# Optimization experiments

Measured on AMD Instinct MI355X. Metric: run time of the kernel, lower is better.

Reference implementation:

```python
import jax, jax.numpy as jnp
import numpy as np

D_MODEL = 2048
NUM_HEADS = 32
NUM_KV_HEADS = 8
HEAD_DIM = D_MODEL // NUM_HEADS  # 64
KV_DIM = NUM_KV_HEADS * HEAD_DIM  # 512


def setup_inputs() -> dict:
    key = jax.random.key(0)
    ks = jax.random.split(key, 9)
    s = 1.0 / np.sqrt(D_MODEL)
    x = jax.random.normal(ks[0], (4, 1024, D_MODEL), dtype=jnp.float32)
    Wq = jax.random.uniform(ks[1], (D_MODEL, D_MODEL), jnp.float32, -s, s)
    bq = jax.random.uniform(ks[2], (D_MODEL,), jnp.float32, -s, s)
    Wk = jax.random.uniform(ks[3], (D_MODEL, KV_DIM), jnp.float32, -s, s)
    bk = jax.random.uniform(ks[4], (KV_DIM,), jnp.float32, -s, s)
    Wv = jax.random.uniform(ks[5], (D_MODEL, KV_DIM), jnp.float32, -s, s)
    bv = jax.random.uniform(ks[6], (KV_DIM,), jnp.float32, -s, s)
    Wo = jax.random.uniform(ks[7], (D_MODEL, D_MODEL), jnp.float32, -s, s)
    bo = jax.random.uniform(ks[8], (D_MODEL,), jnp.float32, -s, s)
    return {"x": x, "Wq": Wq, "bq": bq, "Wk": Wk, "bk": bk,
            "Wv": Wv, "bv": bv, "Wo": Wo, "bo": bo}


def reference(x, Wq, bq, Wk, bk, Wv, bv, Wo, bo):
    B, S, _ = x.shape
    g = NUM_HEADS // NUM_KV_HEADS  # heads per kv head
    # projections
    q = (x @ Wq + bq).reshape(B, S, NUM_HEADS, HEAD_DIM).transpose(0, 2, 1, 3)   # [B,H,S,d]
    k = (x @ Wk + bk).reshape(B, S, NUM_KV_HEADS, HEAD_DIM).transpose(0, 2, 1, 3)  # [B,Hkv,S,d]
    v = (x @ Wv + bv).reshape(B, S, NUM_KV_HEADS, HEAD_DIM).transpose(0, 2, 1, 3)
    # repeat_interleave KV heads across query-head groups
    k = jnp.repeat(k, g, axis=1)  # [B,H,S,d]
    v = jnp.repeat(v, g, axis=1)
    scores = jnp.einsum('bhqd,bhkd->bhqk', q, k) / np.sqrt(HEAD_DIM)  # [B,H,S,S]
    attn = jax.nn.softmax(scores, axis=-1)
    ctx = jnp.einsum('bhqk,bhkd->bhqd', attn, v)  # [B,H,S,d]
    ctx = ctx.transpose(0, 2, 1, 3).reshape(B, S, D_MODEL)
    return ctx @ Wo + bo
```

## Files before the change

### kernel.cpp

```cpp
#include <hip/hip_runtime.h>
#include <stdint.h>

typedef unsigned short u16;
typedef __attribute__((ext_vector_type(8))) __bf16 bf16x8;
typedef __attribute__((ext_vector_type(4))) __bf16 bf16x4;
typedef __attribute__((ext_vector_type(4))) float f32x4;

#define QSCALE 0.1803368801111204f

#if __has_builtin(__builtin_amdgcn_exp2f)
#define EXP2(x) __builtin_amdgcn_exp2f(x)
#else
#define EXP2(x) exp2f(x)
#endif

__device__ __forceinline__ u16 f2bf(float f) {
  uint32_t u = __float_as_uint(f);
  u += 0x7fffu + ((u >> 16) & 1u);
  return (u16)(u >> 16);
}
__device__ __forceinline__ float bf2f(u16 h) {
  return __uint_as_float(((uint32_t)h) << 16);
}
__device__ __forceinline__ uint32_t pack2bf(float a, float b) {
  return (uint32_t)f2bf(a) | ((uint32_t)f2bf(b) << 16);
}

__device__ __forceinline__ void gl_lds16(const u16* g, u16* l) {
  __builtin_amdgcn_global_load_lds(
      (const __attribute__((address_space(1))) unsigned int*)g,
      (__attribute__((address_space(3))) unsigned int*)l, 16, 0, 0);
}

#define S_BAR() __builtin_amdgcn_s_barrier()
#define LGKM0() do { __asm__ volatile("s_waitcnt lgkmcnt(0)" ::: "memory"); \
                     __builtin_amdgcn_sched_barrier(0); } while (0)
#define VMC(N) do { __asm__ volatile("s_waitcnt vmcnt(" #N ")" ::: "memory"); \
                    __builtin_amdgcn_sched_barrier(0); } while (0)

__global__ void detect_dtype(const u16* __restrict__ x, int* __restrict__ flag) {
  __shared__ int any_huge;
  if (threadIdx.x == 0) any_huge = 0;
  __syncthreads();
  int huge = 0;
  for (int i = threadIdx.x; i < 4096; i += 256) {
    float v = bf2f(x[i]);
    if (!(fabsf(v) < 1e6f)) huge = 1;
  }
  if (huge) any_huge = 1;
  __syncthreads();
  if (threadIdx.x == 0) *flag = any_huge;
}

__global__ __launch_bounds__(256) void prep(
    const void* __restrict__ Wq, const void* __restrict__ Wk,
    const void* __restrict__ Wv, const void* __restrict__ Wo,
    const void* __restrict__ x,
    const void* __restrict__ bq, const void* __restrict__ bk,
    const void* __restrict__ bv, const void* __restrict__ bo,
    u16* __restrict__ WT, u16* __restrict__ WoT, u16* __restrict__ xb,
    float* __restrict__ biasf, const int* __restrict__ flag) {
  const int fl = *flag;
  int id = blockIdx.x;
  const int tid = threadIdx.x;
  if (id < 2560) {
    __shared__ u16 tile[64 * 72];
    const void* in; u16* outp; int N, rowoff;
    if (id < 1024)      { in = Wq; outp = WT;  N = 2048; rowoff = 0; }
    else if (id < 1280) { in = Wk; outp = WT;  N = 512;  rowoff = 2048; id -= 1024; }
    else if (id < 1536) { in = Wv; outp = WT;  N = 512;  rowoff = 2560; id -= 1280; }
    else                { in = Wo; outp = WoT; N = 2048; rowoff = 0;    id -= 1536; }
    int tiles_x = N >> 6;
    int nb = (id % tiles_x) * 64, kb = (id / tiles_x) * 64;
    const int kbase = (tid >> 4) * 4, nc = (tid & 15) * 4;
    if (fl) {
      float4 L[4];
#pragma unroll
      for (int p = 0; p < 4; ++p)
        L[p] = *(const float4*)&((const float*)in)[(size_t)(kb + kbase + p) * N + nb + nc];
#pragma unroll
      for (int nj = 0; nj < 4; ++nj) {
        uint2 w;
        w.x = pack2bf(((const float*)&L[0])[nj], ((const float*)&L[1])[nj]);
        w.y = pack2bf(((const float*)&L[2])[nj], ((const float*)&L[3])[nj]);
        *(uint2*)&tile[(nc + nj) * 72 + kbase] = w;
      }
    } else {
      uint2 L[4];
#pragma unroll
      for (int p = 0; p < 4; ++p)
        L[p] = *(const uint2*)&((const u16*)in)[(size_t)(kb + kbase + p) * N + nb + nc];
#pragma unroll
      for (int nj = 0; nj < 4; ++nj) {
        uint2 w;
        w.x = (uint32_t)((const u16*)&L[0])[nj] | ((uint32_t)((const u16*)&L[1])[nj] << 16);
        w.y = (uint32_t)((const u16*)&L[2])[nj] | ((uint32_t)((const u16*)&L[3])[nj] << 16);
        *(uint2*)&tile[(nc + nj) * 72 + kbase] = w;
      }
    }
    __syncthreads();
#pragma unroll
    for (int it = 0; it < 2; ++it) {
      int sid = it * 256 + tid;
      int row = sid >> 3, kseg = (sid & 7) * 8;
      uint4 v = *(const uint4*)&tile[row * 72 + kseg];
      *(uint4*)&outp[(size_t)(rowoff + nb + row) * 2048 + kb + kseg] = v;
    }
  } else if (id < 4608) {
    size_t base = ((size_t)(id - 2560) * 256 + tid) * 16;
    if (fl) {
      const float* xf = (const float*)x;
      float4 a = *(const float4*)&xf[base];
      float4 b = *(const float4*)&xf[base + 4];
      float4 c = *(const float4*)&xf[base + 8];
      float4 d = *(const float4*)&xf[base + 12];
      uint4 o0, o1;
      o0.x = pack2bf(a.x, a.y); o0.y = pack2bf(a.z, a.w);
      o0.z = pack2bf(b.x, b.y); o0.w = pack2bf(b.z, b.w);
      o1.x = pack2bf(c.x, c.y); o1.y = pack2bf(c.z, c.w);
      o1.z = pack2bf(d.x, d.y); o1.w = pack2bf(d.z, d.w);
      *(uint4*)&xb[base] = o0;
      *(uint4*)&xb[base + 8] = o1;
    } else {
      const u16* x16 = (const u16*)x;
      *(uint4*)&xb[base] = *(const uint4*)&x16[base];
      *(uint4*)&xb[base + 8] = *(const uint4*)&x16[base + 8];
    }
  } else {
    int i = (id - 4608) * 256 + tid;
    if (i < 5120) {
      const void* src; int idx;
      if (i < 2048)      { src = bq; idx = i; }
      else if (i < 2560) { src = bk; idx = i - 2048; }
      else if (i < 3072) { src = bv; idx = i - 2560; }
      else               { src = bo; idx = i - 3072; }
      biasf[i] = fl ? ((const float*)src)[idx] : bf2f(((const u16*)src)[idx]);
    }
  }
}

template <bool SWAP>
__device__ __forceinline__ void gemm_loop256(
    const u16* __restrict__ gA, const u16* __restrict__ gB,
    u16* __restrict__ lds, int tid, f32x4 (&acc)[8][4]) {
  const int wave = tid >> 6, lane = tid & 63;
  const int ln = lane & 15, quad = lane >> 4;
  const int sw8 = 8 * (quad ^ ((ln >> 1) & 3));
  const int wm = (wave >> 2) * 128, wn = (wave & 3) * 64;

  u16* const A0b = lds;
  u16* const A1b = lds + 16384;
  u16* const B0b = lds + 32768;
  u16* const B1b = lds + 49152;

  const int srow = wave * 16 + (lane >> 2);
  const int skq = 8 * ((lane & 3) ^ ((lane >> 3) & 3));
  const u16* const sa = gA + (size_t)srow * 2048 + skq;
  const u16* const sb = gB + (size_t)srow * 2048 + skq;
  const int dchunk = (wave * 64 + lane) * 8;

  auto stage = [&](const u16* g, u16* dbase, int H, int kt) {
    const u16* s = g + (size_t)H * (128 * 2048) + kt;
    u16* d = dbase + H * 4096 + dchunk;
    gl_lds16(s, d);
    gl_lds16(s + 32, d + 8192);
  };

  bf16x8 af0[8], af1[8], blo[4], bhi[4];
  auto rdA = [&](bf16x8* dst, const u16* buf, int ibase) {
#pragma unroll
    for (int ii = 0; ii < 4; ++ii) {
      const int ro = (wm + (ibase + ii) * 16 + ln) * 32 + sw8;
      dst[ii * 2 + 0] = *(const bf16x8*)&buf[ro];
      dst[ii * 2 + 1] = *(const bf16x8*)&buf[8192 + ro];
    }
  };
  auto rdB = [&](bf16x8* dst, const u16* buf, int jbase) {
#pragma unroll
    for (int jj = 0; jj < 2; ++jj) {
      const int ro = (wn + (jbase + jj) * 16 + ln) * 32 + sw8;
      dst[jj * 2 + 0] = *(const bf16x8*)&buf[ro];
      dst[jj * 2 + 1] = *(const bf16x8*)&buf[8192 + ro];
    }
  };
  auto mmaQ = [&](int i0, int j0, const bf16x8* a, const bf16x8* b) {
#pragma unroll
    for (int ii = 0; ii < 4; ++ii)
#pragma unroll
      for (int jj = 0; jj < 2; ++jj)
#pragma unroll
        for (int kh = 0; kh < 2; ++kh) {
          f32x4& c = acc[i0 + ii][j0 + jj];
          c = SWAP ? __builtin_amdgcn_mfma_f32_16x16x32_bf16(b[jj * 2 + kh], a[ii * 2 + kh], c, 0, 0, 0)
                   : __builtin_amdgcn_mfma_f32_16x16x32_bf16(a[ii * 2 + kh], b[jj * 2 + kh], c, 0, 0, 0);
        }
  };

  stage(sa, A0b, 0, 0); stage(sa, A0b, 1, 0);
  stage(sb, B0b, 0, 0); stage(sb, B0b, 1, 0);
  stage(sa, A1b, 0, 64); stage(sa, A1b, 1, 64);
  __asm__ volatile("s_waitcnt vmcnt(4)" ::: "memory");
  S_BAR();

#pragma unroll 1
  for (int it = 0; it < 16; ++it) {
    const int kk = it * 128;
#pragma unroll
    for (int h = 0; h < 2; ++h) {
      u16* const Ab = h ? A1b : A0b;
      u16* const Bb = h ? B1b : B0b;
      u16* const Bo = h ? B0b : B1b;
      const int kB = (kk + 64 + h * 64) & 2047;
      const int kA = (kk + 128 + h * 64) & 2047;
      rdA(af0, Ab, 0); rdB(blo, Bb, 0);
      stage(sb, Bo, 0, kB);
      S_BAR(); LGKM0();
      __builtin_amdgcn_s_setprio(1); mmaQ(0, 0, af0, blo); __builtin_amdgcn_s_setprio(0);
      S_BAR();
      rdA(af1, Ab, 4);
      stage(sb, Bo, 1, kB);
      S_BAR(); LGKM0();
      __builtin_amdgcn_s_setprio(1); mmaQ(4, 0, af1, blo); __builtin_amdgcn_s_setprio(0);
      S_BAR();
      rdB(bhi, Bb, 2);
      stage(sa, Ab, 0, kA);
      S_BAR(); LGKM0();
      __builtin_amdgcn_s_setprio(1); mmaQ(4, 2, af1, bhi); __builtin_amdgcn_s_setprio(0);
      S_BAR();
      stage(sa, Ab, 1, kA);
      S_BAR();
      __builtin_amdgcn_s_setprio(1); mmaQ(0, 2, af0, bhi); __builtin_amdgcn_s_setprio(0);
      VMC(4);
      S_BAR();
    }
  }
}

__global__ __launch_bounds__(512, 2) void gemm_qkv(
    const u16* __restrict__ A, const u16* __restrict__ BT,
    const float* __restrict__ bias,
    u16* __restrict__ qo, u16* __restrict__ ko, u16* __restrict__ vo) {
  __shared__ __align__(16) u16 lds[65536];
  const int tid = threadIdx.x;
  const int wave = tid >> 6, lane = tid & 63;
  const int ln = lane & 15, quad = lane >> 4;
  const int wm = (wave >> 2) * 128, wn = (wave & 3) * 64;
  const int m0 = blockIdx.y * 256, n0 = blockIdx.x * 256;

  f32x4 acc[8][4];
#pragma unroll
  for (int i = 0; i < 8; ++i)
#pragma unroll
    for (int j = 0; j < 4; ++j) acc[i][j] = {0.f, 0.f, 0.f, 0.f};

  if (blockIdx.x < 10) {
    gemm_loop256<true>(A + (size_t)m0 * 2048, BT + (size_t)n0 * 2048, lds, tid, acc);
    const bool isq = (n0 < 2048);
    u16* const o = isq ? qo : ko;
    const int hmul = isq ? 32 : 8;
#pragma unroll
    for (int j = 0; j < 4; ++j) {
      const int nbase = n0 + wn + j * 16 + quad * 4;
      const float4 bsv = *(const float4*)&bias[nbase];
      const int n2 = isq ? nbase : nbase - 2048;
      const int hh = n2 >> 6, dd = n2 & 63;
#pragma unroll
      for (int i = 0; i < 8; ++i) {
        const int m = m0 + wm + i * 16 + ln;
        const int b = m >> 10, s = m & 1023;
        float v0 = acc[i][j][0] + bsv.x, v1 = acc[i][j][1] + bsv.y;
        float v2 = acc[i][j][2] + bsv.z, v3 = acc[i][j][3] + bsv.w;
        if (isq) { v0 *= QSCALE; v1 *= QSCALE; v2 *= QSCALE; v3 *= QSCALE; }
        uint2 st; st.x = pack2bf(v0, v1); st.y = pack2bf(v2, v3);
        *(uint2*)&o[(((size_t)(b * hmul + hh)) * 1024 + s) * 64 + dd] = st;
      }
    }
  } else {
    gemm_loop256<false>(A + (size_t)m0 * 2048, BT + (size_t)n0 * 2048, lds, tid, acc);
#pragma unroll
    for (int j = 0; j < 4; ++j) {
      const int gn = n0 + wn + j * 16 + ln;
      const float bs = bias[gn];
      const int n2 = gn - 2560, hh = n2 >> 6, dd = n2 & 63;
#pragma unroll
      for (int i = 0; i < 8; ++i) {
        const int mb = m0 + wm + i * 16 + quad * 4;
        const int b = mb >> 10, sb = mb & 1023;
        uint2 st;
        st.x = pack2bf(acc[i][j][0] + bs, acc[i][j][1] + bs);
        st.y = pack2bf(acc[i][j][2] + bs, acc[i][j][3] + bs);
        *(uint2*)&vo[(((size_t)(b * 8 + hh)) * 64 + dd) * 1024 + sb] = st;
      }
    }
  }
}

__global__ __launch_bounds__(512, 2) void gemm_o(
    const u16* __restrict__ A, const u16* __restrict__ BT,
    const float* __restrict__ bias, u16* __restrict__ o0,
    const int* __restrict__ flag) {
  __shared__ __align__(16) u16 lds[65536];
  const int tid = threadIdx.x;
  const int wave = tid >> 6, lane = tid & 63;
  const int ln = lane & 15, quad = lane >> 4;
  const int wm = (wave >> 2) * 128, wn = (wave & 3) * 64;
  const int m0 = blockIdx.y * 256, n0 = blockIdx.x * 256;
  const int fl = *flag;

  f32x4 acc[8][4];
#pragma unroll
  for (int i = 0; i < 8; ++i)
#pragma unroll
    for (int j = 0; j < 4; ++j) acc[i][j] = {0.f, 0.f, 0.f, 0.f};

  gemm_loop256<true>(A + (size_t)m0 * 2048, BT + (size_t)n0 * 2048, lds, tid, acc);

#pragma unroll
  for (int j = 0; j < 4; ++j) {
    const int nbase = n0 + wn + j * 16 + quad * 4;
    const float4 bsv = *(const float4*)&bias[nbase];
#pragma unroll
    for (int i = 0; i < 8; ++i) {
      const int m = m0 + wm + i * 16 + ln;
      float v0 = acc[i][j][0] + bsv.x, v1 = acc[i][j][1] + bsv.y;
      float v2 = acc[i][j][2] + bsv.z, v3 = acc[i][j][3] + bsv.w;
      if (fl) {
        float4 st = {v0, v1, v2, v3};
        *(float4*)&((float*)o0)[(size_t)m * 2048 + nbase] = st;
      } else {
        uint2 st; st.x = pack2bf(v0, v1); st.y = pack2bf(v2, v3);
        *(uint2*)&o0[(size_t)m * 2048 + nbase] = st;
      }
    }
  }
}

__global__ __launch_bounds__(256) void attn_kernel(
    const u16* __restrict__ q_ws, const u16* __restrict__ k_ws,
    const u16* __restrict__ vt_ws, u16* __restrict__ ctx) {
  __shared__ u16 Kl[64 * 72];
  __shared__ u16 Vl[64 * 72];
  __shared__ u16 Pl[4 * 16 * 68];
  const int tid = threadIdx.x;
  const int wave = tid >> 6, lane = tid & 63;
  const int ln = lane & 15, quad = lane >> 4;
  const int qt = blockIdx.x;
  const int bh = blockIdx.y;
  const int b = bh >> 5, h = bh & 31, kvh = h >> 2;
  const int q0 = qt * 64;
  const size_t qbase = (size_t)bh * 1024 * 64;
  const u16* kptr = k_ws + (size_t)(b * 8 + kvh) * 1024 * 64;
  const u16* vptr = vt_ws + (size_t)(b * 8 + kvh) * 64 * 1024;

  const int qrow = q0 + wave * 16 + ln;
  bf16x8 qf0 = *(const bf16x8*)&q_ws[qbase + (size_t)qrow * 64 + quad * 8];
  bf16x8 qf1 = *(const bf16x8*)&q_ws[qbase + (size_t)qrow * 64 + 32 + quad * 8];

  float lsum = 0.f;
  f32x4 oacc[4];
#pragma unroll
  for (int t = 0; t < 4; ++t) oacc[t] = {0.f, 0.f, 0.f, 0.f};

  const int kr0 = tid >> 3, kp0 = (tid & 7) * 8;
  const int kr1 = kr0 + 32;
  const int prow = wave * 16 * 68 + ln * 68;

  uint4 kv0 = *(const uint4*)&kptr[(size_t)kr0 * 64 + kp0];
  uint4 kv1 = *(const uint4*)&kptr[(size_t)kr1 * 64 + kp0];
  uint4 vv0 = *(const uint4*)&vptr[(size_t)kr0 * 1024 + kp0];
  uint4 vv1 = *(const uint4*)&vptr[(size_t)kr1 * 1024 + kp0];

  for (int kb = 0; kb < 1024; kb += 64) {
    __syncthreads();
    *(uint4*)&Kl[kr0 * 72 + kp0] = kv0;
    *(uint4*)&Kl[kr1 * 72 + kp0] = kv1;
    *(uint4*)&Vl[kr0 * 72 + kp0] = vv0;
    *(uint4*)&Vl[kr1 * 72 + kp0] = vv1;
    __syncthreads();

    {
      int nkb = (kb + 64) & 1023;
      kv0 = *(const uint4*)&kptr[(size_t)(nkb + kr0) * 64 + kp0];
      kv1 = *(const uint4*)&kptr[(size_t)(nkb + kr1) * 64 + kp0];
      vv0 = *(const uint4*)&vptr[(size_t)kr0 * 1024 + nkb + kp0];
      vv1 = *(const uint4*)&vptr[(size_t)kr1 * 1024 + nkb + kp0];
    }

    f32x4 sacc[4];
#pragma unroll
    for (int t = 0; t < 4; ++t) sacc[t] = {0.f, 0.f, 0.f, 0.f};
#pragma unroll
    for (int t = 0; t < 4; ++t) {
      bf16x8 kf0 = *(const bf16x8*)&Kl[(t * 16 + ln) * 72 + quad * 8];
      bf16x8 kf1 = *(const bf16x8*)&Kl[(t * 16 + ln) * 72 + 32 + quad * 8];
      sacc[t] = __builtin_amdgcn_mfma_f32_16x16x32_bf16(kf0, qf0, sacc[t], 0, 0, 0);
      sacc[t] = __builtin_amdgcn_mfma_f32_16x16x32_bf16(kf1, qf1, sacc[t], 0, 0, 0);
    }

    uint2 pk[4];
#pragma unroll
    for (int t = 0; t < 4; ++t) {
      float p0 = EXP2(sacc[t][0]);
      float p1 = EXP2(sacc[t][1]);
      float p2 = EXP2(sacc[t][2]);
      float p3 = EXP2(sacc[t][3]);
      lsum += (p0 + p1) + (p2 + p3);
      pk[t].x = __builtin_amdgcn_perm(__float_as_uint(p1), __float_as_uint(p0), 0x07060302u);
      pk[t].y = __builtin_amdgcn_perm(__float_as_uint(p3), __float_as_uint(p2), 0x07060302u);
    }
#pragma unroll
    for (int t = 0; t < 4; ++t)
      *(uint2*)&Pl[prow + t * 16 + quad * 4] = pk[t];
    __asm__ volatile("s_waitcnt lgkmcnt(0)" ::: "memory");

    bf16x8 pf0 = *(const bf16x8*)&Pl[prow + quad * 8];
    bf16x8 pf1 = *(const bf16x8*)&Pl[prow + 32 + quad * 8];

#pragma unroll
    for (int t = 0; t < 4; ++t) {
      bf16x8 vf0 = *(const bf16x8*)&Vl[(t * 16 + ln) * 72 + quad * 8];
      bf16x8 vf1 = *(const bf16x8*)&Vl[(t * 16 + ln) * 72 + 32 + quad * 8];
      oacc[t] = __builtin_amdgcn_mfma_f32_16x16x32_bf16(vf0, pf0, oacc[t], 0, 0, 0);
      oacc[t] = __builtin_amdgcn_mfma_f32_16x16x32_bf16(vf1, pf1, oacc[t], 0, 0, 0);
    }
  }

  float l2 = lsum + __shfl_xor(lsum, 16);
  l2 += __shfl_xor(l2, 32);
  const float inv = 1.0f / l2;

  const size_t obase = (size_t)(b * 1024 + qrow) * 2048 + h * 64;
#pragma unroll
  for (int t = 0; t < 4; ++t) {
    uint2 st;
    st.x = pack2bf(oacc[t][0] * inv, oacc[t][1] * inv);
    st.y = pack2bf(oacc[t][2] * inv, oacc[t][3] * inv);
    *(uint2*)&ctx[obase + t * 16 + quad * 4] = st;
  }
}

extern "C" void kernel_launch(void* const* d_in, const int* in_sizes, int n_in,
                              void* d_out, int out_size, void* d_ws, size_t ws_size,
                              hipStream_t stream) {
  const void* x  = d_in[0];
  const void* Wq = d_in[1];
  const void* bq = d_in[2];
  const void* Wk = d_in[3];
  const void* bk = d_in[4];
  const void* Wv = d_in[5];
  const void* bv = d_in[6];
  const void* Wo = d_in[7];
  const void* bo = d_in[8];
  char* ws = (char*)d_ws;

  u16* WT    = (u16*)(ws + 0);
  u16* WoT   = (u16*)(ws + 12582912);
  u16* q_ws  = (u16*)(ws + 20971520);
  u16* k_ws  = (u16*)(ws + 37748736);
  u16* vt_ws = (u16*)(ws + 41943040);
  u16* c_ws  = (u16*)(ws + 46137344);
  u16* xb    = (u16*)(ws + 62914560);
  float* biasf = (float*)(ws + 79691776);
  int* flag  = (int*)(ws + 79712256);

  detect_dtype<<<1, 256, 0, stream>>>((const u16*)x, flag);
  prep<<<4628, 256, 0, stream>>>(Wq, Wk, Wv, Wo, x, bq, bk, bv, bo,
                                 WT, WoT, xb, biasf, flag);

  gemm_qkv<<<dim3(12, 16), 512, 0, stream>>>(xb, WT, biasf, q_ws, k_ws, vt_ws);
  attn_kernel<<<dim3(16, 128), 256, 0, stream>>>(q_ws, k_ws, vt_ws, c_ws);
  gemm_o<<<dim3(8, 16), 512, 0, stream>>>(c_ws, WoT, biasf + 3072, (u16*)d_out, flag);
}
```

Before: 294.3 us.

## Retile QKV and output GEMMs to smaller tiles for better CU occupancy

Replaces the shared 256x256 GEMM main loop with per-kernel variants. The QKV projection now uses 128x384 tiles on a 8x32 grid, and the output projection uses 256x128 tiles on a 16x16 grid. Both raise the block count (192 to 256, 128 to 256) so the 256 CUs are filled instead of partly idle. In exchange each tile reuses less data per load, and the V epilogue now writes transposed output as scalar 16-bit stores instead of packed stores.

Result: faster. 277.0 us (-5.9%).

```diff
diff --git a/kernel.cpp b/kernel.cpp
--- a/kernel.cpp
+++ b/kernel.cpp
@@ -139,103 +139,6 @@
   }
 }
 
-template <bool SWAP>
-__device__ __forceinline__ void gemm_loop256(
-    const u16* __restrict__ gA, const u16* __restrict__ gB,
-    u16* __restrict__ lds, int tid, f32x4 (&acc)[8][4]) {
-  const int wave = tid >> 6, lane = tid & 63;
-  const int ln = lane & 15, quad = lane >> 4;
-  const int sw8 = 8 * (quad ^ ((ln >> 1) & 3));
-  const int wm = (wave >> 2) * 128, wn = (wave & 3) * 64;
-
-  u16* const A0b = lds;
-  u16* const A1b = lds + 16384;
-  u16* const B0b = lds + 32768;
-  u16* const B1b = lds + 49152;
-
-  const int srow = wave * 16 + (lane >> 2);
-  const int skq = 8 * ((lane & 3) ^ ((lane >> 3) & 3));
-  const u16* const sa = gA + (size_t)srow * 2048 + skq;
-  const u16* const sb = gB + (size_t)srow * 2048 + skq;
-  const int dchunk = (wave * 64 + lane) * 8;
-
-  auto stage = [&](const u16* g, u16* dbase, int H, int kt) {
-    const u16* s = g + (size_t)H * (128 * 2048) + kt;
-    u16* d = dbase + H * 4096 + dchunk;
-    gl_lds16(s, d);
-    gl_lds16(s + 32, d + 8192);
-  };
-
-  bf16x8 af0[8], af1[8], blo[4], bhi[4];
-  auto rdA = [&](bf16x8* dst, const u16* buf, int ibase) {
-#pragma unroll
-    for (int ii = 0; ii < 4; ++ii) {
-      const int ro = (wm + (ibase + ii) * 16 + ln) * 32 + sw8;
-      dst[ii * 2 + 0] = *(const bf16x8*)&buf[ro];
-      dst[ii * 2 + 1] = *(const bf16x8*)&buf[8192 + ro];
-    }
-  };
-  auto rdB = [&](bf16x8* dst, const u16* buf, int jbase) {
-#pragma unroll
-    for (int jj = 0; jj < 2; ++jj) {
-      const int ro = (wn + (jbase + jj) * 16 + ln) * 32 + sw8;
-      dst[jj * 2 + 0] = *(const bf16x8*)&buf[ro];
-      dst[jj * 2 + 1] = *(const bf16x8*)&buf[8192 + ro];
-    }
-  };
-  auto mmaQ = [&](int i0, int j0, const bf16x8* a, const bf16x8* b) {
-#pragma unroll
-    for (int ii = 0; ii < 4; ++ii)
-#pragma unroll
-      for (int jj = 0; jj < 2; ++jj)
-#pragma unroll
-        for (int kh = 0; kh < 2; ++kh) {
-          f32x4& c = acc[i0 + ii][j0 + jj];
-          c = SWAP ? __builtin_amdgcn_mfma_f32_16x16x32_bf16(b[jj * 2 + kh], a[ii * 2 + kh], c, 0, 0, 0)
-                   : __builtin_amdgcn_mfma_f32_16x16x32_bf16(a[ii * 2 + kh], b[jj * 2 + kh], c, 0, 0, 0);
-        }
-  };
-
-  stage(sa, A0b, 0, 0); stage(sa, A0b, 1, 0);
-  stage(sb, B0b, 0, 0); stage(sb, B0b, 1, 0);
-  stage(sa, A1b, 0, 64); stage(sa, A1b, 1, 64);
-  __asm__ volatile("s_waitcnt vmcnt(4)" ::: "memory");
-  S_BAR();
-
-#pragma unroll 1
-  for (int it = 0; it < 16; ++it) {
-    const int kk = it * 128;
-#pragma unroll
-    for (int h = 0; h < 2; ++h) {
-      u16* const Ab = h ? A1b : A0b;
-      u16* const Bb = h ? B1b : B0b;
-      u16* const Bo = h ? B0b : B1b;
-      const int kB = (kk + 64 + h * 64) & 2047;
-      const int kA = (kk + 128 + h * 64) & 2047;
-      rdA(af0, Ab, 0); rdB(blo, Bb, 0);
-      stage(sb, Bo, 0, kB);
-      S_BAR(); LGKM0();
-      __builtin_amdgcn_s_setprio(1); mmaQ(0, 0, af0, blo); __builtin_amdgcn_s_setprio(0);
-      S_BAR();
-      rdA(af1, Ab, 4);
-      stage(sb, Bo, 1, kB);
-      S_BAR(); LGKM0();
-      __builtin_amdgcn_s_setprio(1); mmaQ(4, 0, af1, blo); __builtin_amdgcn_s_setprio(0);
-      S_BAR();
-      rdB(bhi, Bb, 2);
-      stage(sa, Ab, 0, kA);
-      S_BAR(); LGKM0();
-      __builtin_amdgcn_s_setprio(1); mmaQ(4, 2, af1, bhi); __builtin_amdgcn_s_setprio(0);
-      S_BAR();
-      stage(sa, Ab, 1, kA);
-      S_BAR();
-      __builtin_amdgcn_s_setprio(1); mmaQ(0, 2, af0, bhi); __builtin_amdgcn_s_setprio(0);
-      VMC(4);
-      S_BAR();
-    }
-  }
-}
-
 __global__ __launch_bounds__(512, 2) void gemm_qkv(
     const u16* __restrict__ A, const u16* __restrict__ BT,
     const float* __restrict__ bias,
@@ -244,52 +147,138 @@
   const int tid = threadIdx.x;
   const int wave = tid >> 6, lane = tid & 63;
   const int ln = lane & 15, quad = lane >> 4;
-  const int wm = (wave >> 2) * 128, wn = (wave & 3) * 64;
-  const int m0 = blockIdx.y * 256, n0 = blockIdx.x * 256;
-
-  f32x4 acc[8][4];
+  const int sw8 = 8 * (quad ^ ((ln >> 1) & 3));
+  const int m0 = blockIdx.y * 128, n0 = blockIdx.x * 384;
+
+  u16* const A0b = lds;
+  u16* const A1b = lds + 8192;
+  u16* const B0b = lds + 16384;
+  u16* const B1b = lds + 40960;
+
+  const int srow = wave * 16 + (lane >> 2);
+  const int skq = 8 * ((lane & 3) ^ ((lane >> 3) & 3));
+  const u16* const sa = A + (size_t)(m0 + srow) * 2048 + skq;
+  const u16* const sb = BT + (size_t)(n0 + srow) * 2048 + skq;
+  const int dc8 = (wave * 64 + lane) * 8;
+
+  auto stageA = [&](u16* dbase, int kt) {
+    const u16* s = sa + kt;
+    gl_lds16(s, dbase + dc8);
+    gl_lds16(s + 32, dbase + dc8 + 4096);
+  };
+  auto stageB = [&](u16* dbase, int u, int kt) {
+    const u16* s = sb + (size_t)u * 262144 + kt;
+    u16* d = dbase + u * 4096 + dc8;
+    gl_lds16(s, d);
+    gl_lds16(s + 32, d + 12288);
+  };
+
+  f32x4 acc[8][3];
 #pragma unroll
   for (int i = 0; i < 8; ++i)
 #pragma unroll
-    for (int j = 0; j < 4; ++j) acc[i][j] = {0.f, 0.f, 0.f, 0.f};
-
-  if (blockIdx.x < 10) {
-    gemm_loop256<true>(A + (size_t)m0 * 2048, BT + (size_t)n0 * 2048, lds, tid, acc);
-    const bool isq = (n0 < 2048);
-    u16* const o = isq ? qo : ko;
-    const int hmul = isq ? 32 : 8;
-#pragma unroll
-    for (int j = 0; j < 4; ++j) {
-      const int nbase = n0 + wn + j * 16 + quad * 4;
-      const float4 bsv = *(const float4*)&bias[nbase];
-      const int n2 = isq ? nbase : nbase - 2048;
-      const int hh = n2 >> 6, dd = n2 & 63;
+    for (int j = 0; j < 3; ++j) acc[i][j] = {0.f, 0.f, 0.f, 0.f};
+
+  bf16x8 aL[8], aH[8], b0f[2], b1f[2], b2f[2];
+  auto rdAh = [&](bf16x8* dst, const u16* buf, int ibase) {
+#pragma unroll
+    for (int ii = 0; ii < 4; ++ii) {
+      const int ro = ((ibase + ii) * 16 + ln) * 32 + sw8;
+      dst[ii * 2 + 0] = *(const bf16x8*)&buf[ro];
+      dst[ii * 2 + 1] = *(const bf16x8*)&buf[ro + 4096];
+    }
+  };
+  auto rdBj = [&](bf16x8* dst, const u16* buf, int j) {
+    const int ro = (wave * 48 + j * 16 + ln) * 32 + sw8;
+    dst[0] = *(const bf16x8*)&buf[ro];
+    dst[1] = *(const bf16x8*)&buf[ro + 12288];
+  };
+  auto mma8 = [&](const bf16x8* a4, const bf16x8* bj, int ibase, int j) {
+#pragma unroll
+    for (int ii = 0; ii < 4; ++ii)
+#pragma unroll
+      for (int kh = 0; kh < 2; ++kh)
+        acc[ibase + ii][j] = __builtin_amdgcn_mfma_f32_16x16x32_bf16(
+            bj[kh], a4[ii * 2 + kh], acc[ibase + ii][j], 0, 0, 0);
+  };
+
+  stageA(A0b, 0);
+  stageB(B0b, 0, 0); stageB(B0b, 1, 0); stageB(B0b, 2, 0);
+  stageA(A1b, 64);
+  __asm__ volatile("s_waitcnt vmcnt(2)" ::: "memory");
+  S_BAR();
+
+#pragma unroll 1
+  for (int it = 0; it < 16; ++it) {
+    const int kk = it * 128;
+#pragma unroll
+    for (int h = 0; h < 2; ++h) {
+      u16* const Ab = h ? A1b : A0b;
+      u16* const Bb = h ? B1b : B0b;
+      u16* const Bo = h ? B0b : B1b;
+      const int kB = (kk + 64 + h * 64) & 2047;
+      const int kA = (kk + 128 + h * 64) & 2047;
+      rdAh(aL, Ab, 0); rdBj(b0f, Bb, 0);
+      stageB(Bo, 0, kB);
+      S_BAR(); LGKM0();
+      __builtin_amdgcn_s_setprio(1); mma8(aL, b0f, 0, 0); __builtin_amdgcn_s_setprio(0);
+      S_BAR();
+      rdAh(aH, Ab, 4); rdBj(b1f, Bb, 1);
+      stageB(Bo, 1, kB);
+      S_BAR(); LGKM0();
+      __builtin_amdgcn_s_setprio(1); mma8(aH, b0f, 4, 0); mma8(aL, b1f, 0, 1); __builtin_amdgcn_s_setprio(0);
+      S_BAR();
+      rdBj(b2f, Bb, 2);
+      stageB(Bo, 2, kB);
+      S_BAR(); LGKM0();
+      __builtin_amdgcn_s_setprio(1); mma8(aH, b1f, 4, 1); mma8(aL, b2f, 0, 2); __builtin_amdgcn_s_setprio(0);
+      S_BAR();
+      stageA(Ab, kA);
+      S_BAR();
+      __builtin_amdgcn_s_setprio(1); mma8(aH, b2f, 4, 2); __builtin_amdgcn_s_setprio(0);
+      VMC(2);
+      S_BAR();
+    }
+  }
+
+#pragma unroll
+  for (int j = 0; j < 3; ++j) {
+    const int gnf = n0 + wave * 48 + j * 16;
+    const int gn = gnf + quad * 4;
+    const float4 bsv = *(const float4*)&bias[gn];
+    if (gnf < 2048) {
+      const int hh = gn >> 6, dd = gn & 63;
 #pragma unroll
       for (int i = 0; i < 8; ++i) {
-        const int m = m0 + wm + i * 16 + ln;
+        const int m = m0 + i * 16 + ln;
         const int b = m >> 10, s = m & 1023;
-        float v0 = acc[i][j][0] + bsv.x, v1 = acc[i][j][1] + bsv.y;
-        float v2 = acc[i][j][2] + bsv.z, v3 = acc[i][j][3] + bsv.w;
-        if (isq) { v0 *= QSCALE; v1 *= QSCALE; v2 *= QSCALE; v3 *= QSCALE; }
-        uint2 st; st.x = pack2bf(v0, v1); st.y = pack2bf(v2, v3);
-        *(uint2*)&o[(((size_t)(b * hmul + hh)) * 1024 + s) * 64 + dd] = st;
+        uint2 st;
+        st.x = pack2bf((acc[i][j][0] + bsv.x) * QSCALE, (acc[i][j][1] + bsv.y) * QSCALE);
+        st.y = pack2bf((acc[i][j][2] + bsv.z) * QSCALE, (acc[i][j][3] + bsv.w) * QSCALE);
+        *(uint2*)&qo[(((size_t)(b * 32 + hh)) * 1024 + s) * 64 + dd] = st;
       }
-    }
-  } else {
-    gemm_loop256<false>(A + (size_t)m0 * 2048, BT + (size_t)n0 * 2048, lds, tid, acc);
-#pragma unroll
-    for (int j = 0; j < 4; ++j) {
-      const int gn = n0 + wn + j * 16 + ln;
-      const float bs = bias[gn];
-      const int n2 = gn - 2560, hh = n2 >> 6, dd = n2 & 63;
+    } else if (gnf < 2560) {
+      const int n2 = gn - 2048, hh = n2 >> 6, dd = n2 & 63;
 #pragma unroll
       for (int i = 0; i < 8; ++i) {
-        const int mb = m0 + wm + i * 16 + quad * 4;
-        const int b = mb >> 10, sb = mb & 1023;
+        const int m = m0 + i * 16 + ln;
+        const int b = m >> 10, s = m & 1023;
         uint2 st;
-        st.x = pack2bf(acc[i][j][0] + bs, acc[i][j][1] + bs);
-        st.y = pack2bf(acc[i][j][2] + bs, acc[i][j][3] + bs);
-        *(uint2*)&vo[(((size_t)(b * 8 + hh)) * 64 + dd) * 1024 + sb] = st;
+        st.x = pack2bf(acc[i][j][0] + bsv.x, acc[i][j][1] + bsv.y);
+        st.y = pack2bf(acc[i][j][2] + bsv.z, acc[i][j][3] + bsv.w);
+        *(uint2*)&ko[(((size_t)(b * 8 + hh)) * 1024 + s) * 64 + dd] = st;
+      }
+    } else {
+      const int n2 = gn - 2560, hh = n2 >> 6, dd0 = n2 & 63;
+#pragma unroll
+      for (int i = 0; i < 8; ++i) {
+        const int m = m0 + i * 16 + ln;
+        const int b = m >> 10, s = m & 1023;
+        const size_t vb = ((size_t)(b * 8 + hh) * 64 + dd0) * 1024 + s;
+        vo[vb]        = f2bf(acc[i][j][0] + bsv.x);
+        vo[vb + 1024] = f2bf(acc[i][j][1] + bsv.y);
+        vo[vb + 2048] = f2bf(acc[i][j][2] + bsv.z);
+        vo[vb + 3072] = f2bf(acc[i][j][3] + bsv.w);
       }
     }
   }
@@ -299,24 +288,106 @@
     const u16* __restrict__ A, const u16* __restrict__ BT,
     const float* __restrict__ bias, u16* __restrict__ o0,
     const int* __restrict__ flag) {
-  __shared__ __align__(16) u16 lds[65536];
+  __shared__ __align__(16) u16 lds[49152];
   const int tid = threadIdx.x;
   const int wave = tid >> 6, lane = tid & 63;
   const int ln = lane & 15, quad = lane >> 4;
-  const int wm = (wave >> 2) * 128, wn = (wave & 3) * 64;
-  const int m0 = blockIdx.y * 256, n0 = blockIdx.x * 256;
+  const int sw8 = 8 * (quad ^ ((ln >> 1) & 3));
+  const int wm = (wave >> 2) * 128, wn = (wave & 3) * 32;
+  const int m0 = blockIdx.y * 256, n0 = blockIdx.x * 128;
   const int fl = *flag;
 
-  f32x4 acc[8][4];
+  u16* const A0b = lds;
+  u16* const A1b = lds + 16384;
+  u16* const B0b = lds + 32768;
+  u16* const B1b = lds + 40960;
+
+  const int srow = wave * 16 + (lane >> 2);
+  const int skq = 8 * ((lane & 3) ^ ((lane >> 3) & 3));
+  const u16* const sa = A + (size_t)(m0 + srow) * 2048 + skq;
+  const u16* const sb = BT + (size_t)(n0 + srow) * 2048 + skq;
+  const int dc8 = (wave * 64 + lane) * 8;
+
+  auto stageA = [&](u16* dbase, int H, int kt) {
+    const u16* s = sa + (size_t)H * 262144 + kt;
+    u16* d = dbase + H * 4096 + dc8;
+    gl_lds16(s, d);
+    gl_lds16(s + 32, d + 8192);
+  };
+  auto stageB = [&](u16* dbase, int kt) {
+    const u16* s = sb + kt;
+    gl_lds16(s, dbase + dc8);
+    gl_lds16(s + 32, dbase + dc8 + 4096);
+  };
+
+  f32x4 acc[8][2];
 #pragma unroll
   for (int i = 0; i < 8; ++i)
 #pragma unroll
-    for (int j = 0; j < 4; ++j) acc[i][j] = {0.f, 0.f, 0.f, 0.f};
-
-  gemm_loop256<true>(A + (size_t)m0 * 2048, BT + (size_t)n0 * 2048, lds, tid, acc);
-
-#pragma unroll
-  for (int j = 0; j < 4; ++j) {
+    for (int j = 0; j < 2; ++j) acc[i][j] = {0.f, 0.f, 0.f, 0.f};
+
+  bf16x8 aL[8], aH[8], b0f[2], b1f[2];
+  auto rdAh = [&](bf16x8* dst, const u16* buf, int ibase) {
+#pragma unroll
+    for (int ii = 0; ii < 4; ++ii) {
+      const int ro = (wm + (ibase + ii) * 16 + ln) * 32 + sw8;
+      dst[ii * 2 + 0] = *(const bf16x8*)&buf[ro];
+      dst[ii * 2 + 1] = *(const bf16x8*)&buf[ro + 8192];
+    }
+  };
+  auto rdBj = [&](bf16x8* dst, const u16* buf, int j) {
+    const int ro = (wn + j * 16 + ln) * 32 + sw8;
+    dst[0] = *(const bf16x8*)&buf[ro];
+    dst[1] = *(const bf16x8*)&buf[ro + 4096];
+  };
+  auto mma8 = [&](const bf16x8* a4, const bf16x8* bj, int ibase, int j) {
+#pragma unroll
+    for (int ii = 0; ii < 4; ++ii)
+#pragma unroll
+      for (int kh = 0; kh < 2; ++kh)
+        acc[ibase + ii][j] = __builtin_amdgcn_mfma_f32_16x16x32_bf16(
+            bj[kh], a4[ii * 2 + kh], acc[ibase + ii][j], 0, 0, 0);
+  };
+
+  stageA(A0b, 0, 0); stageA(A0b, 1, 0);
+  stageB(B0b, 0);
+  stageA(A1b, 0, 64); stageA(A1b, 1, 64);
+  __asm__ volatile("s_waitcnt vmcnt(4)" ::: "memory");
+  S_BAR();
+
+#pragma unroll 1
+  for (int it = 0; it < 16; ++it) {
+    const int kk = it * 128;
+#pragma unroll
+    for (int h = 0; h < 2; ++h) {
+      u16* const Ab = h ? A1b : A0b;
+      u16* const Bb = h ? B1b : B0b;
+      u16* const Bo = h ? B0b : B1b;
+      const int kB = (kk + 64 + h * 64) & 2047;
+      const int kA = (kk + 128 + h * 64) & 2047;
+      rdAh(aL, Ab, 0); rdBj(b0f, Bb, 0);
+      stageB(Bo, kB);
+      S_BAR(); LGKM0();
+      __builtin_amdgcn_s_setprio(1); mma8(aL, b0f, 0, 0); __builtin_amdgcn_s_setprio(0);
+      S_BAR();
+      rdAh(aH, Ab, 4); rdBj(b1f, Bb, 1);
+      S_BAR(); LGKM0();
+      __builtin_amdgcn_s_setprio(1); mma8(aH, b0f, 4, 0); __builtin_amdgcn_s_setprio(0);
+      S_BAR();
+      stageA(Ab, 0, kA);
+      S_BAR();
+      __builtin_amdgcn_s_setprio(1); mma8(aH, b1f, 4, 1); __builtin_amdgcn_s_setprio(0);
+      S_BAR();
+      stageA(Ab, 1, kA);
+      S_BAR();
+      __builtin_amdgcn_s_setprio(1); mma8(aL, b1f, 0, 1); __builtin_amdgcn_s_setprio(0);
+      VMC(4);
+      S_BAR();
+    }
+  }
+
+#pragma unroll
+  for (int j = 0; j < 2; ++j) {
     const int nbase = n0 + wn + j * 16 + quad * 4;
     const float4 bsv = *(const float4*)&bias[nbase];
 #pragma unroll
@@ -467,7 +538,7 @@
   prep<<<4628, 256, 0, stream>>>(Wq, Wk, Wv, Wo, x, bq, bk, bv, bo,
                                  WT, WoT, xb, biasf, flag);
 
-  gemm_qkv<<<dim3(12, 16), 512, 0, stream>>>(xb, WT, biasf, q_ws, k_ws, vt_ws);
+  gemm_qkv<<<dim3(8, 32), 512, 0, stream>>>(xb, WT, biasf, q_ws, k_ws, vt_ws);
   attn_kernel<<<dim3(16, 128), 256, 0, stream>>>(q_ws, k_ws, vt_ws, c_ws);
-  gemm_o<<<dim3(8, 16), 512, 0, stream>>>(c_ws, WoT, biasf + 3072, (u16*)d_out, flag);
-}
+  gemm_o<<<dim3(16, 16), 512, 0, stream>>>(c_ws, WoT, biasf + 3072, (u16*)d_out, flag);
+}
```
